# Kernel tuning notes

Measured on AMD Instinct MI355X. Metric: run time of the kernel, lower is better.

The kernel has to match this reference:

```python
import jax, jax.numpy as jnp
import numpy as np

B, T, C, H, E, K = 2, 2048, 1024, 16, 8, 2
HD = C // H  # 64
FF = 4 * C   # 4096


def _ln(x, g, b, eps=1e-5):
    m = x.mean(-1, keepdims=True)
    v = x.var(-1, keepdims=True)
    return (x - m) / jnp.sqrt(v + eps) * g + b


def setup_inputs() -> dict:
    key = jax.random.key(0)
    ks = jax.random.split(key, 12)
    s = 0.02
    return {
        "x": jax.random.normal(ks[0], (B, T, C), jnp.float32),
        "Wq": jax.random.normal(ks[1], (H, C, HD), jnp.float32) * s,
        "Wk": jax.random.normal(ks[2], (H, C, HD), jnp.float32) * s,
        "Wv": jax.random.normal(ks[3], (H, C, HD), jnp.float32) * s,
        "Wo": jax.random.normal(ks[4], (C, C), jnp.float32) * s,
        "bo": jnp.zeros((C,), jnp.float32),
        "ln1_g": jnp.ones((C,), jnp.float32),
        "ln1_b": jnp.zeros((C,), jnp.float32),
        "Wr": jax.random.normal(ks[5], (C, E), jnp.float32) * s,
        "br": jnp.zeros((E,), jnp.float32),
        "Wn": jax.random.normal(ks[6], (C, E), jnp.float32) * s,
        "bn": jnp.zeros((E,), jnp.float32),
        "W1": jax.random.normal(ks[7], (E, C, FF), jnp.float32) * s,
        "b1": jnp.zeros((E, FF), jnp.float32),
        "W2": jax.random.normal(ks[8], (E, FF, C), jnp.float32) * s,
        "b2": jnp.zeros((E, C), jnp.float32),
        "ln2_g": jnp.ones((C,), jnp.float32),
        "ln2_b": jnp.zeros((C,), jnp.float32),
        "noise": jax.random.normal(ks[9], (B, T, E), jnp.float32),
    }


def reference(x, Wq, Wk, Wv, Wo, bo, ln1_g, ln1_b, Wr, br, Wn, bn,
              W1, b1, W2, b2, ln2_g, ln2_b, noise):
    # --- multi-head causal attention (note: scale uses full C, faithful to source) ---
    q = jnp.einsum('btc,hcd->bhtd', x, Wq)
    k = jnp.einsum('btc,hcd->bhtd', x, Wk)
    v = jnp.einsum('btc,hcd->bhtd', x, Wv)
    wei = jnp.einsum('bhtd,bhsd->bhts', q, k) * (C ** -0.5)
    mask = jnp.tril(jnp.ones((T, T), bool))
    wei = jnp.where(mask, wei, -jnp.inf)
    wei = jax.nn.softmax(wei, axis=-1)
    attn = jnp.einsum('bhts,bhsd->bhtd', wei, v)
    attn = attn.transpose(0, 2, 1, 3).reshape(B, T, C)  # concat heads
    attn = attn @ Wo + bo  # proj (dropout = identity in eval)
    x1 = x + _ln(attn, ln1_g, ln1_b)

    # --- noisy top-k router ---
    logits = x1 @ Wr + br                          # [B,T,E]
    noise_logits = x1 @ Wn + bn
    noisy = logits + noise * jax.nn.softplus(noise_logits)
    top_vals, top_idx = jax.lax.top_k(noisy, K)    # [B,T,K]
    # softmax over -inf-filled sparse logits == softmax over the top-k values,
    # scattered back to expert slots; non-selected experts get exactly 0.
    sm = jax.nn.softmax(top_vals, axis=-1)         # [B,T,K]
    gates = jnp.sum(jax.nn.one_hot(top_idx, E, dtype=x.dtype) * sm[..., None], axis=-2)  # [B,T,E]

    # --- experts: dense grouped FFN, combined with (mostly-zero) gates ---
    h = jnp.einsum('btc,ecf->ebtf', x1, W1) + b1[:, None, None, :]
    h = jax.nn.gelu(h, approximate=False)          # torch nn.GELU default = exact erf
    eo = jnp.einsum('ebtf,efc->ebtc', h, W2) + b2[:, None, None, :]
    moe = jnp.einsum('ebtc,bte->btc', eo, gates)

    return x1 + _ln(moe, ln2_g, ln2_b)
```

## Files before the change

### kernel.cpp

```cpp
#include <hip/hip_runtime.h>
#include <math.h>

constexpr int BB = 2, TT = 2048, CC = 1024, HH = 16, HD = 64, EE = 8, FF = 4096;
constexpr int BT = BB * TT;
constexpr int FFC = 2048;

constexpr size_t W = (size_t)BT * CC;
constexpr size_t OFF_Q    = 0;
constexpr size_t OFF_K    = W;
constexpr size_t OFF_V    = 2 * W;
constexpr size_t SM_BASE  = 3 * W;
constexpr size_t SM_GATES = SM_BASE;
constexpr size_t SM_EIDS  = SM_BASE + 8192;
constexpr size_t SM_STOK  = SM_BASE + 16384;
constexpr size_t SM_SGATE = SM_BASE + 24576;
constexpr size_t SM_CNT   = SM_BASE + 32768;
constexpr size_t SM_OFFS  = SM_BASE + 32776;
constexpr size_t SM_CUR   = SM_BASE + 32784;
constexpr size_t SM_ACNT  = SM_BASE + 32792;

typedef short bf16x8 __attribute__((ext_vector_type(8)));
typedef float f32x4  __attribute__((ext_vector_type(4)));

__device__ __forceinline__ float gelu_exact(float v) {
    return 0.5f * v * (1.0f + erff(v * 0.70710678118654752440f));
}

__device__ __forceinline__ short f2bf(float f) {
    unsigned u = __float_as_uint(f);
    unsigned r = 0x7fffu + ((u >> 16) & 1u);
    return (short)((u + r) >> 16);
}

__device__ __forceinline__ bf16x8 pack8(float4 a, float4 b) {
    bf16x8 o;
    o[0] = f2bf(a.x); o[1] = f2bf(a.y); o[2] = f2bf(a.z); o[3] = f2bf(a.w);
    o[4] = f2bf(b.x); o[5] = f2bf(b.y); o[6] = f2bf(b.z); o[7] = f2bf(b.w);
    return o;
}

__device__ __forceinline__ void f4a(float4 v, float* a) {
    a[0] = v.x; a[1] = v.y; a[2] = v.z; a[3] = v.w;
}

__device__ __forceinline__ int SW(int r, int c4) {
    return (((c4 >> 2) ^ ((r >> 2) & 15)) << 2);
}

__device__ __forceinline__ void sgemm128_core(const float* __restrict__ ap,
                                              const float* __restrict__ bp0,
                                              const float* __restrict__ bp1,
                                              long bks, int Kd, float acc[8][8],
                                              float (*As)[128], float (*Bs)[128]) {
    const int t    = threadIdx.x;
    const int kb   = (t & 1) << 3;
    const int mrow = t >> 1;
    const int kq   = t >> 4;
    const int c16  = (t & 15) << 2;
    const int tr4  = (t >> 4) << 2, tc4 = (t & 15) << 2;
    float4 a0 = *(const float4*)(ap + kb);
    float4 a1 = *(const float4*)(ap + kb + 4);
    float4 b0 = *(const float4*)(bp0);
    float4 b1 = *(const float4*)(bp1);
    for (int k0 = 0; k0 < Kd; k0 += 16) {
        __syncthreads();
        As[kb + 0][mrow] = a0.x; As[kb + 1][mrow] = a0.y;
        As[kb + 2][mrow] = a0.z; As[kb + 3][mrow] = a0.w;
        As[kb + 4][mrow] = a1.x; As[kb + 5][mrow] = a1.y;
        As[kb + 6][mrow] = a1.z; As[kb + 7][mrow] = a1.w;
        *(float4*)&Bs[kq][c16]      = b0;
        *(float4*)&Bs[kq][c16 + 64] = b1;
        __syncthreads();
        if (k0 + 16 < Kd) {
            a0 = *(const float4*)(ap + k0 + 16 + kb);
            a1 = *(const float4*)(ap + k0 + 16 + kb + 4);
            b0 = *(const float4*)(bp0 + (size_t)(k0 + 16) * bks);
            b1 = *(const float4*)(bp1 + (size_t)(k0 + 16) * bks);
        }
#pragma unroll
        for (int kk = 0; kk < 16; ++kk) {
            float av[8], bv[8];
            f4a(*(const float4*)&As[kk][tr4],      av);
            f4a(*(const float4*)&As[kk][tr4 + 64], av + 4);
            f4a(*(const float4*)&Bs[kk][tc4],      bv);
            f4a(*(const float4*)&Bs[kk][tc4 + 64], bv + 4);
#pragma unroll
            for (int i = 0; i < 8; ++i)
#pragma unroll
                for (int j = 0; j < 8; ++j)
                    acc[i][j] = fmaf(av[i], bv[j], acc[i][j]);
        }
    }
}

__global__ __launch_bounds__(256) void qkv_kernel(const float* __restrict__ x,
                                                  const float* __restrict__ Wq,
                                                  const float* __restrict__ Wk,
                                                  const float* __restrict__ Wv,
                                                  float* __restrict__ q,
                                                  float* __restrict__ k,
                                                  float* __restrict__ v) {
    __shared__ float As[16][128], Bs[16][128];
    const int mt = blockIdx.x, nt = blockIdx.y, wz = blockIdx.z;
    const float* Wm = (wz == 0) ? Wq : ((wz == 1) ? Wk : Wv);
    float* out = (wz == 0) ? q : ((wz == 1) ? k : v);
    const int t = threadIdx.x;
    const int kq = t >> 4, c16 = (t & 15) << 2;
    const float* ap  = x + (size_t)(mt * 128 + (t >> 1)) * CC;
    const float* bp0 = Wm + ((size_t)(2 * nt)     * CC + kq) * HD + c16;
    const float* bp1 = Wm + ((size_t)(2 * nt + 1) * CC + kq) * HD + c16;
    float acc[8][8] = {};
    sgemm128_core(ap, bp0, bp1, HD, CC, acc, As, Bs);
    const int tr4 = (t >> 4) << 2, tc4 = (t & 15) << 2;
#pragma unroll
    for (int i = 0; i < 8; ++i) {
        const int row = mt * 128 + (i >> 2) * 64 + tr4 + (i & 3);
        float4 o0, o1;
        o0.x = acc[i][0]; o0.y = acc[i][1]; o0.z = acc[i][2]; o0.w = acc[i][3];
        o1.x = acc[i][4]; o1.y = acc[i][5]; o1.z = acc[i][6]; o1.w = acc[i][7];
        *(float4*)&out[(size_t)row * CC + nt * 128 + tc4]      = o0;
        *(float4*)&out[(size_t)row * CC + nt * 128 + 64 + tc4] = o1;
    }
}

__global__ __launch_bounds__(256) void gemm_bias_kernel(const float* __restrict__ A,
                                                        const float* __restrict__ Bm,
                                                        const float* __restrict__ bias,
                                                        float* __restrict__ out,
                                                        int N, int Kd) {
    __shared__ float As[16][128], Bs[16][128];
    const int mt = blockIdx.x, nt = blockIdx.y;
    const int t = threadIdx.x;
    const int kq = t >> 4, c16 = (t & 15) << 2;
    const float* ap  = A + (size_t)(mt * 128 + (t >> 1)) * Kd;
    const float* bp0 = Bm + (size_t)kq * N + nt * 128 + c16;
    const float* bp1 = bp0 + 64;
    float acc[8][8] = {};
    sgemm128_core(ap, bp0, bp1, N, Kd, acc, As, Bs);
    const int tr4 = (t >> 4) << 2, tc4 = (t & 15) << 2;
    const float4 ba = *(const float4*)&bias[nt * 128 + tc4];
    const float4 bb = *(const float4*)&bias[nt * 128 + 64 + tc4];
#pragma unroll
    for (int i = 0; i < 8; ++i) {
        const int row = mt * 128 + (i >> 2) * 64 + tr4 + (i & 3);
        float4 o0, o1;
        o0.x = acc[i][0] + ba.x; o0.y = acc[i][1] + ba.y;
        o0.z = acc[i][2] + ba.z; o0.w = acc[i][3] + ba.w;
        o1.x = acc[i][4] + bb.x; o1.y = acc[i][5] + bb.y;
        o1.z = acc[i][6] + bb.z; o1.w = acc[i][7] + bb.w;
        *(float4*)&out[(size_t)row * N + nt * 128 + tc4]      = o0;
        *(float4*)&out[(size_t)row * N + nt * 128 + 64 + tc4] = o1;
    }
}

constexpr int ATTN_JOBS = (TT / 64) * HH * BB;
__global__ __launch_bounds__(256) void attn_kernel(float* __restrict__ q,
                                                   const float* __restrict__ kbuf,
                                                   const float* __restrict__ vbuf,
                                                   int* __restrict__ jctr) {
    __shared__ float Qs[64][64];
    __shared__ float Ks[64][64];
    __shared__ float Vs[64][64];
    __shared__ int jid_s;
    float (*Ps)[64] = Ks;
    const int t = threadIdx.x;
    const int tc4 = (t & 15) << 2, tr4 = (t >> 4) << 2;
    for (;;) {
        __syncthreads();
        if (t == 0) jid_s = atomicAdd(jctr, 1);
        __syncthreads();
        const int jid = jid_s;
        if (jid >= ATTN_JOBS) break;
        const int qt    = (TT / 64 - 1) - (jid >> 5);
        const int plane = jid & 31;
        const int h = plane & 15, b = plane >> 4;
        const size_t base = ((size_t)b * TT) * CC + h * HD;
#pragma unroll
        for (int it = 0; it < 4; ++it) {
            int fi = t + it * 256;
            int r = fi >> 4, c4 = (fi & 15) << 2;
            *(float4*)&Qs[r][SW(r, c4)] =
                *(const float4*)&q[base + (size_t)(qt * 64 + r) * CC + c4];
        }
        float4 kr[4], vr[4];
#pragma unroll
        for (int it = 0; it < 4; ++it) {
            int fi = t + it * 256;
            int s = fi >> 4, c4 = (fi & 15) << 2;
            kr[it] = *(const float4*)&kbuf[base + (size_t)s * CC + c4];
            vr[it] = *(const float4*)&vbuf[base + (size_t)s * CC + c4];
        }
        float o[4][4] = {};
        float m_r[4], l_r[4];
#pragma unroll
        for (int i = 0; i < 4; ++i) { m_r[i] = -INFINITY; l_r[i] = 0.0f; }

        for (int kt = 0; kt <= qt; ++kt) {
            __syncthreads();
#pragma unroll
            for (int it = 0; it < 4; ++it) {
                int fi = t + it * 256;
                int s = fi >> 4, c4 = (fi & 15) << 2;
                *(float4*)&Ks[s][SW(s, c4)] = kr[it];
                *(float4*)&Vs[s][SW(s, c4)] = vr[it];
            }
            __syncthreads();
            if (kt < qt) {
#pragma unroll
                for (int it = 0; it < 4; ++it) {
                    int fi = t + it * 256;
                    int s = fi >> 4, c4 = (fi & 15) << 2;
                    kr[it] = *(const float4*)&kbuf[base + (size_t)((kt + 1) * 64 + s) * CC + c4];
                    vr[it] = *(const float4*)&vbuf[base + (size_t)((kt + 1) * 64 + s) * CC + c4];
                }
            }
            float s4[4][4] = {};
            for (int d4 = 0; d4 < 64; d4 += 4) {
                float qa[4][4], ka[4][4];
#pragma unroll
                for (int i = 0; i < 4; ++i)
                    f4a(*(const float4*)&Qs[tr4 + i][SW(tr4 + i, d4)], qa[i]);
#pragma unroll
                for (int j = 0; j < 4; ++j)
                    f4a(*(const float4*)&Ks[tc4 + j][SW(tc4 + j, d4)], ka[j]);
#pragma unroll
                for (int i = 0; i < 4; ++i)
#pragma unroll
                    for (int j = 0; j < 4; ++j) {
                        float a = s4[i][j];
                        a = fmaf(qa[i][0], ka[j][0], a);
                        a = fmaf(qa[i][1], ka[j][1], a);
                        a = fmaf(qa[i][2], ka[j][2], a);
                        a = fmaf(qa[i][3], ka[j][3], a);
                        s4[i][j] = a;
                    }
            }
            const float scale = 0.03125f;
#pragma unroll
            for (int i = 0; i < 4; ++i)
#pragma unroll
                for (int j = 0; j < 4; ++j) {
                    float sv = s4[i][j] * scale;
                    if (kt == qt && (tc4 + j) > (tr4 + i)) sv = -INFINITY;
                    s4[i][j] = sv;
                }
            float p4[4][4];
#pragma unroll
            for (int i = 0; i < 4; ++i) {
                float mt_i = fmaxf(fmaxf(s4[i][0], s4[i][1]), fmaxf(s4[i][2], s4[i][3]));
#pragma unroll
                for (int msk = 1; msk <= 8; msk <<= 1) mt_i = fmaxf(mt_i, __shfl_xor(mt_i, msk, 64));
                float m_new = fmaxf(m_r[i], mt_i);
                float alpha = expf(m_r[i] - m_new);
                float ls = 0.0f;
#pragma unroll
                for (int j = 0; j < 4; ++j) {
                    float p = expf(s4[i][j] - m_new);
                    p4[i][j] = p;
                    ls += p;
                }
#pragma unroll
                for (int msk = 1; msk <= 8; msk <<= 1) ls += __shfl_xor(ls, msk, 64);
                l_r[i] = l_r[i] * alpha + ls;
                m_r[i] = m_new;
#pragma unroll
                for (int j = 0; j < 4; ++j) o[i][j] *= alpha;
            }
            __syncthreads();
#pragma unroll
            for (int i = 0; i < 4; ++i) {
                float4 pv;
                pv.x = p4[i][0]; pv.y = p4[i][1]; pv.z = p4[i][2]; pv.w = p4[i][3];
                *(float4*)&Ps[tr4 + i][SW(tr4 + i, tc4)] = pv;
            }
            __syncthreads();
            for (int s0 = 0; s0 < 64; s0 += 4) {
                float pa[4][4], va[4][4];
#pragma unroll
                for (int i = 0; i < 4; ++i)
                    f4a(*(const float4*)&Ps[tr4 + i][SW(tr4 + i, s0)], pa[i]);
#pragma unroll
                for (int qq = 0; qq < 4; ++qq)
                    f4a(*(const float4*)&Vs[s0 + qq][SW(s0 + qq, tc4)], va[qq]);
#pragma unroll
                for (int i = 0; i < 4; ++i)
#pragma unroll
                    for (int j = 0; j < 4; ++j) {
                        float a = o[i][j];
                        a = fmaf(pa[i][0], va[0][j], a);
                        a = fmaf(pa[i][1], va[1][j], a);
                        a = fmaf(pa[i][2], va[2][j], a);
                        a = fmaf(pa[i][3], va[3][j], a);
                        o[i][j] = a;
                    }
            }
        }
#pragma unroll
        for (int i = 0; i < 4; ++i) {
            const float inv = 1.0f / l_r[i];
            float4 o4;
            o4.x = o[i][0] * inv; o4.y = o[i][1] * inv; o4.z = o[i][2] * inv; o4.w = o[i][3] * inv;
            *(float4*)&q[base + (size_t)(qt * 64 + tr4 + i) * CC + tc4] = o4;
        }
    }
}

__device__ __forceinline__ void compute_step(short (*As)[40], short (*Bs)[40],
                                             f32x4 acc[4][4], int wm, int wn,
                                             int l15, int q8) {
    bf16x8 a[4], b[4];
#pragma unroll
    for (int i = 0; i < 4; ++i) a[i] = *(bf16x8*)&As[wm + i * 16 + l15][q8];
#pragma unroll
    for (int j = 0; j < 4; ++j) b[j] = *(bf16x8*)&Bs[wn + j * 16 + l15][q8];
#pragma unroll
    for (int i = 0; i < 4; ++i)
#pragma unroll
        for (int j = 0; j < 4; ++j)
            acc[i][j] = __builtin_amdgcn_mfma_f32_16x16x32_bf16(a[i], b[j], acc[i][j], 0, 0, 0);
}

#define MM_PROLOG                                                    \
    const int t = threadIdx.x, lane = t & 63, wid = t >> 6;          \
    const int wm = (wid >> 1) * 64, wn = (wid & 1) * 64;             \
    const int l15 = lane & 15, q8 = (lane >> 4) * 8;                 \
    const int arow = t >> 1, akh = (t & 1) * 16;                     \
    const int bn = t & 127, bkh = (t >> 7) * 16;

__global__ __launch_bounds__(256) void mm_ffn1(const float* __restrict__ x1,
                                               const float* __restrict__ W1,
                                               const float* __restrict__ b1,
                                               const int* __restrict__ stok,
                                               const int* __restrict__ offs,
                                               const int* __restrict__ cnt,
                                               short* __restrict__ hbuf, int fbase) {
    __shared__ short As[128][40], Bs[128][40];
    const int e = blockIdx.z, mt = blockIdx.x, nt = blockIdx.y;
    const int ne = cnt[e];
    if (mt * 128 >= ne) return;
    MM_PROLOG
    const int off_e = offs[e];
    int rl = mt * 128 + arow;
    if (rl >= ne) rl = ne - 1;
    const int token = stok[off_e + rl];
    const float* ap = x1 + (size_t)token * CC;
    const float* bp = W1 + (size_t)e * CC * FF + fbase + nt * 128 + bn;
    f32x4 acc[4][4] = {};
    float4 apf[4];
    float bpf[16];
#pragma unroll
    for (int qd = 0; qd < 4; ++qd) apf[qd] = *(const float4*)(ap + akh + 4 * qd);
#pragma unroll
    for (int kk = 0; kk < 16; ++kk) bpf[kk] = bp[(size_t)(bkh + kk) * FF];
    for (int k0 = 0; k0 < CC; k0 += 32) {
        __syncthreads();
        *(bf16x8*)&As[arow][akh]     = pack8(apf[0], apf[1]);
        *(bf16x8*)&As[arow][akh + 8] = pack8(apf[2], apf[3]);
        {
            bf16x8 o0, o1;
#pragma unroll
            for (int kk = 0; kk < 8; ++kk) { o0[kk] = f2bf(bpf[kk]); o1[kk] = f2bf(bpf[kk + 8]); }
            *(bf16x8*)&Bs[bn][bkh]     = o0;
            *(bf16x8*)&Bs[bn][bkh + 8] = o1;
        }
        __syncthreads();
        if (k0 + 32 < CC) {
#pragma unroll
            for (int qd = 0; qd < 4; ++qd)
                apf[qd] = *(const float4*)(ap + k0 + 32 + akh + 4 * qd);
#pragma unroll
            for (int kk = 0; kk < 16; ++kk)
                bpf[kk] = bp[(size_t)(k0 + 32 + bkh + kk) * FF];
        }
        compute_step(As, Bs, acc, wm, wn, l15, q8);
    }
    float bj[4];
#pragma unroll
    for (int j = 0; j < 4; ++j)
        bj[j] = b1[(size_t)e * FF + fbase + nt * 128 + wn + j * 16 + l15];
    const int colb = nt * 128 + wn;
#pragma unroll
    for (int i = 0; i < 4; ++i) {
#pragma unroll
        for (int r = 0; r < 4; ++r) {
            const int row = mt * 128 + wm + i * 16 + (lane >> 4) * 4 + r;
            if (row < ne) {
                short* orow = hbuf + (size_t)(off_e + row) * FFC + colb;
#pragma unroll
                for (int j = 0; j < 4; ++j)
                    orow[j * 16 + l15] = f2bf(gelu_exact(acc[i][j][r] + bj[j]));
            }
        }
    }
}

__global__ __launch_bounds__(256) void mm_ffn2(const short* __restrict__ hbuf,
                                               const float* __restrict__ W2,
                                               const float* __restrict__ b2,
                                               const int* __restrict__ stok,
                                               const float* __restrict__ sgate,
                                               const int* __restrict__ offs,
                                               const int* __restrict__ cnt,
                                               float* __restrict__ moe,
                                               int fbase, int first) {
    __shared__ short As[128][40], Bs[128][40];
    const int e = blockIdx.z, mt = blockIdx.x, nt = blockIdx.y;
    const int ne = cnt[e];
    if (mt * 128 >= ne) return;
    MM_PROLOG
    const int off_e = offs[e];
    int rl = mt * 128 + arow;
    if (rl >= ne) rl = ne - 1;
    const short* ap = hbuf + (size_t)(off_e + rl) * FFC;
    const float* bp = W2 + (size_t)e * FF * CC + (size_t)fbase * CC + nt * 128 + bn;
    f32x4 acc[4][4] = {};
    bf16x8 a0pf = *(const bf16x8*)(ap + akh);
    bf16x8 a1pf = *(const bf16x8*)(ap + akh + 8);
    float bpf[16];
#pragma unroll
    for (int kk = 0; kk < 16; ++kk) bpf[kk] = bp[(size_t)(bkh + kk) * CC];
    for (int k0 = 0; k0 < FFC; k0 += 32) {
        __syncthreads();
        *(bf16x8*)&As[arow][akh]     = a0pf;
        *(bf16x8*)&As[arow][akh + 8] = a1pf;
        {
            bf16x8 o0, o1;
#pragma unroll
            for (int kk = 0; kk < 8; ++kk) { o0[kk] = f2bf(bpf[kk]); o1[kk] = f2bf(bpf[kk + 8]); }
            *(bf16x8*)&Bs[bn][bkh]     = o0;
            *(bf16x8*)&Bs[bn][bkh + 8] = o1;
        }
        __syncthreads();
        if (k0 + 32 < FFC) {
            a0pf = *(const bf16x8*)(ap + k0 + 32 + akh);
            a1pf = *(const bf16x8*)(ap + k0 + 32 + akh + 8);
#pragma unroll
            for (int kk = 0; kk < 16; ++kk)
                bpf[kk] = bp[(size_t)(k0 + 32 + bkh + kk) * CC];
        }
        compute_step(As, Bs, acc, wm, wn, l15, q8);
    }
    float bj[4];
    int colj[4];
#pragma unroll
    for (int j = 0; j < 4; ++j) {
        colj[j] = nt * 128 + wn + j * 16 + l15;
        bj[j] = first ? b2[(size_t)e * CC + colj[j]] : 0.0f;
    }
#pragma unroll
    for (int i = 0; i < 4; ++i) {
#pragma unroll
        for (int r = 0; r < 4; ++r) {
            const int row = mt * 128 + wm + i * 16 + (lane >> 4) * 4 + r;
            if (row < ne) {
                const int slot = off_e + row;
                const int token = stok[slot];
                const float g = sgate[slot];
                float* dst = moe + (size_t)token * CC;
#pragma unroll
                for (int j = 0; j < 4; ++j)
                    atomicAdd(dst + colj[j], g * (acc[i][j][r] + bj[j]));
            }
        }
    }
}

__device__ __forceinline__ float block_sum(float v, float* red) {
#pragma unroll
    for (int m = 32; m >= 1; m >>= 1) v += __shfl_xor(v, m, 64);
    const int w = threadIdx.x >> 6;
    __syncthreads();
    if ((threadIdx.x & 63) == 0) red[w] = v;
    __syncthreads();
    return red[0] + red[1] + red[2] + red[3];
}

__global__ __launch_bounds__(256) void ln_res_kernel(const float* __restrict__ src,
                                                     const float* __restrict__ res,
                                                     const float* __restrict__ gam,
                                                     const float* __restrict__ bet,
                                                     float* __restrict__ out) {
    __shared__ float red[4];
    const int row = blockIdx.x, t = threadIdx.x;
    const float4 sv = *(const float4*)&src[(size_t)row * CC + t * 4];
    const float total = block_sum(sv.x + sv.y + sv.z + sv.w, red);
    const float mean = total * (1.0f / CC);
    const float d0 = sv.x - mean, d1 = sv.y - mean, d2 = sv.z - mean, d3 = sv.w - mean;
    const float var = block_sum(d0 * d0 + d1 * d1 + d2 * d2 + d3 * d3, red) * (1.0f / CC);
    const float rstd = rsqrtf(var + 1e-5f);
    const float4 rv = *(const float4*)&res[(size_t)row * CC + t * 4];
    const float4 g4 = *(const float4*)&gam[t * 4];
    const float4 b4 = *(const float4*)&bet[t * 4];
    float4 o4;
    o4.x = rv.x + d0 * rstd * g4.x + b4.x;
    o4.y = rv.y + d1 * rstd * g4.y + b4.y;
    o4.z = rv.z + d2 * rstd * g4.z + b4.z;
    o4.w = rv.w + d3 * rstd * g4.w + b4.w;
    *(float4*)&out[(size_t)row * CC + t * 4] = o4;
}

__global__ __launch_bounds__(256) void router_kernel(const float* __restrict__ x1,
                                                     const float* __restrict__ Wr,
                                                     const float* __restrict__ br,
                                                     const float* __restrict__ Wn,
                                                     const float* __restrict__ bn,
                                                     const float* __restrict__ noise,
                                                     float* __restrict__ gates,
                                                     int* __restrict__ eids,
                                                     int* __restrict__ counts) {
    __shared__ float xs[CC];
    __shared__ float part[256];
    __shared__ float dots[16];
    const int tk = blockIdx.x, t = threadIdx.x;
    *(float4*)&xs[t * 4] = *(const float4*)&x1[(size_t)tk * CC + t * 4];
    __syncthreads();
    const int o = t & 15, cs = t >> 4;
    float acc = 0.0f;
    if (o < 8) {
        for (int c = cs; c < CC; c += 16) acc += xs[c] * Wr[c * EE + o];
    } else {
        const int e = o - 8;
        for (int c = cs; c < CC; c += 16) acc += xs[c] * Wn[c * EE + e];
    }
    part[t] = acc;
    __syncthreads();
    if (t < 16) {
        float s = 0.0f;
        for (int i = 0; i < 16; ++i) s += part[t + 16 * i];
        dots[t] = s;
    }
    __syncthreads();
    if (t == 0) {
        float noisy[EE];
        for (int e = 0; e < EE; ++e) {
            const float lg = dots[e] + br[e];
            const float nl = dots[8 + e] + bn[e];
            const float sp = fmaxf(nl, 0.0f) + log1pf(expf(-fabsf(nl)));
            noisy[e] = lg + noise[(size_t)tk * EE + e] * sp;
        }
        int e1 = 0; float v1 = noisy[0];
        for (int e = 1; e < EE; ++e) if (noisy[e] > v1) { v1 = noisy[e]; e1 = e; }
        int e2 = -1; float v2 = -INFINITY;
        for (int e = 0; e < EE; ++e) if (e != e1 && noisy[e] > v2) { v2 = noisy[e]; e2 = e; }
        const float ex = expf(v2 - v1);
        const float inv = 1.0f / (1.0f + ex);
        gates[2 * tk] = inv; gates[2 * tk + 1] = ex * inv;
        eids[2 * tk] = e1; eids[2 * tk + 1] = e2;
        atomicAdd(&counts[e1], 1);
        atomicAdd(&counts[e2], 1);
    }
}

__global__ void zero_counts_kernel(int* __restrict__ cnt, int* __restrict__ acnt) {
    if (threadIdx.x < EE) cnt[threadIdx.x] = 0;
    if (threadIdx.x == EE) *acnt = 0;
}

__global__ void offsets_kernel(const int* __restrict__ cnt, int* __restrict__ offs,
                               int* __restrict__ cur) {
    const int t = threadIdx.x;
    if (t == 0) {
        int a = 0;
        for (int e = 0; e < EE; ++e) { offs[e] = a; a += cnt[e]; }
    }
    if (t < EE) cur[t] = 0;
}

__global__ __launch_bounds__(256) void scatter_kernel(const int* __restrict__ eids,
                                                      const float* __restrict__ gates,
                                                      int* __restrict__ cur,
                                                      const int* __restrict__ offs,
                                                      int* __restrict__ slot_token,
                                                      float* __restrict__ slot_gate) {
    const int tk = blockIdx.x * 256 + threadIdx.x;
    if (tk >= BT) return;
#pragma unroll
    for (int ki = 0; ki < 2; ++ki) {
        const int e = eids[2 * tk + ki];
        const int idx = atomicAdd(&cur[e], 1);
        const int slot = offs[e] + idx;
        slot_token[slot] = tk;
        slot_gate[slot] = gates[2 * tk + ki];
    }
}

__global__ __launch_bounds__(256) void zero_kernel(float* __restrict__ p, int n4) {
    const int i = blockIdx.x * 256 + threadIdx.x;
    if (i < n4) ((float4*)p)[i] = make_float4(0.f, 0.f, 0.f, 0.f);
}

extern "C" void kernel_launch(void* const* d_in, const int* in_sizes, int n_in,
                              void* d_out, int out_size, void* d_ws, size_t ws_size,
                              hipStream_t stream) {
    (void)in_sizes; (void)n_in; (void)out_size; (void)ws_size;
    const float* x    = (const float*)d_in[0];
    const float* Wq   = (const float*)d_in[1];
    const float* Wk   = (const float*)d_in[2];
    const float* Wv   = (const float*)d_in[3];
    const float* Wo   = (const float*)d_in[4];
    const float* bo   = (const float*)d_in[5];
    const float* ln1g = (const float*)d_in[6];
    const float* ln1b = (const float*)d_in[7];
    const float* Wr   = (const float*)d_in[8];
    const float* br   = (const float*)d_in[9];
    const float* Wn   = (const float*)d_in[10];
    const float* bn   = (const float*)d_in[11];
    const float* W1   = (const float*)d_in[12];
    const float* b1   = (const float*)d_in[13];
    const float* W2   = (const float*)d_in[14];
    const float* b2   = (const float*)d_in[15];
    const float* ln2g = (const float*)d_in[16];
    const float* ln2b = (const float*)d_in[17];
    const float* noise= (const float*)d_in[18];
    float* out = (float*)d_out;
    float* ws  = (float*)d_ws;
    int*   iws = (int*)d_ws;

    float* qb    = ws + OFF_Q;
    float* kb    = ws + OFF_K;
    float* vb    = ws + OFF_V;
    float* proj  = ws + OFF_V;
    float* x1    = out;
    short* hbuf  = (short*)(ws + OFF_Q);
    float* moe   = ws + OFF_V;
    float* gates = ws + SM_GATES;
    float* sgate = ws + SM_SGATE;
    int* eids  = iws + SM_EIDS;
    int* stok  = iws + SM_STOK;
    int* cnt   = iws + SM_CNT;
    int* offs  = iws + SM_OFFS;
    int* cur   = iws + SM_CUR;
    int* acnt  = iws + SM_ACNT;

    zero_counts_kernel<<<1, 64, 0, stream>>>(cnt, acnt);
    qkv_kernel<<<dim3(BT / 128, CC / 128, 3), 256, 0, stream>>>(x, Wq, Wk, Wv, qb, kb, vb);
    attn_kernel<<<dim3(768), 256, 0, stream>>>(qb, kb, vb, acnt);
    gemm_bias_kernel<<<dim3(BT / 128, CC / 128), 256, 0, stream>>>(qb, Wo, bo, proj, CC, CC);
    ln_res_kernel<<<BT, 256, 0, stream>>>(proj, x, ln1g, ln1b, x1);
    router_kernel<<<BT, 256, 0, stream>>>(x1, Wr, br, Wn, bn, noise, gates, eids, cnt);
    offsets_kernel<<<1, 64, 0, stream>>>(cnt, offs, cur);
    scatter_kernel<<<BT / 256, 256, 0, stream>>>(eids, gates, cur, offs, stok, sgate);
    zero_kernel<<<(BT * CC / 4 + 255) / 256, 256, 0, stream>>>(moe, BT * CC / 4);
    for (int ccnk = 0; ccnk < FF / FFC; ++ccnk) {
        mm_ffn1<<<dim3(2 * BT / 128, FFC / 128, EE), 256, 0, stream>>>(
            x1, W1, b1, stok, offs, cnt, hbuf, ccnk * FFC);
        mm_ffn2<<<dim3(2 * BT / 128, CC / 128, EE), 256, 0, stream>>>(
            hbuf, W2, b2, stok, sgate, offs, cnt, moe, ccnk * FFC, ccnk == 0 ? 1 : 0);
    }
    ln_res_kernel<<<BT, 256, 0, stream>>>(moe, x1, ln2g, ln2b, out);
}
```

Measured before the change: 2.499 ms.

## Replace atomic scatter-add with per-slot expert output and fused gated combine+LN

The second FFN GEMM now writes its output per routed slot into a dense buffer (store on the first chunk, read-modify-write on later chunks) instead of atomically adding gated results into per-token rows. A new combine kernel gathers each token's two slot rows, applies the gates, and fuses LayerNorm plus residual, so the zero-fill kernel goes away. The scatter kernel records each token's slot indices in place of its expert ids. The FF chunk size is halved to 1024, which doubles the number of GEMM launches and the read-modify-write passes over the expert-output buffer.

```diff
diff --git a/kernel.cpp b/kernel.cpp
--- a/kernel.cpp
+++ b/kernel.cpp
@@ -3,7 +3,7 @@
 
 constexpr int BB = 2, TT = 2048, CC = 1024, HH = 16, HD = 64, EE = 8, FF = 4096;
 constexpr int BT = BB * TT;
-constexpr int FFC = 2048;
+constexpr int FFC = 1024;
 
 constexpr size_t W = (size_t)BT * CC;
 constexpr size_t OFF_Q    = 0;
@@ -397,11 +397,9 @@
 __global__ __launch_bounds__(256) void mm_ffn2(const short* __restrict__ hbuf,
                                                const float* __restrict__ W2,
                                                const float* __restrict__ b2,
-                                               const int* __restrict__ stok,
-                                               const float* __restrict__ sgate,
                                                const int* __restrict__ offs,
                                                const int* __restrict__ cnt,
-                                               float* __restrict__ moe,
+                                               float* __restrict__ eo,
                                                int fbase, int first) {
     __shared__ short As[128][40], Bs[128][40];
     const int e = blockIdx.z, mt = blockIdx.x, nt = blockIdx.y;
@@ -453,13 +451,16 @@
         for (int r = 0; r < 4; ++r) {
             const int row = mt * 128 + wm + i * 16 + (lane >> 4) * 4 + r;
             if (row < ne) {
-                const int slot = off_e + row;
-                const int token = stok[slot];
-                const float g = sgate[slot];
-                float* dst = moe + (size_t)token * CC;
-#pragma unroll
-                for (int j = 0; j < 4; ++j)
-                    atomicAdd(dst + colj[j], g * (acc[i][j][r] + bj[j]));
+                float* dst = eo + (size_t)(off_e + row) * CC;
+                if (first) {
+#pragma unroll
+                    for (int j = 0; j < 4; ++j)
+                        dst[colj[j]] = acc[i][j][r] + bj[j];
+                } else {
+#pragma unroll
+                    for (int j = 0; j < 4; ++j)
+                        dst[colj[j]] += acc[i][j][r];
+                }
             }
         }
     }
@@ -499,6 +500,40 @@
     *(float4*)&out[(size_t)row * CC + t * 4] = o4;
 }
 
+__global__ __launch_bounds__(256) void combine_ln_kernel(const float* __restrict__ eo,
+                                                         const int* __restrict__ tslot,
+                                                         const float* __restrict__ gates,
+                                                         const float* __restrict__ res,
+                                                         const float* __restrict__ gam,
+                                                         const float* __restrict__ bet,
+                                                         float* __restrict__ out) {
+    __shared__ float red[4];
+    const int tk = blockIdx.x, t = threadIdx.x;
+    const int s0 = tslot[2 * tk], s1 = tslot[2 * tk + 1];
+    const float g0 = gates[2 * tk], g1 = gates[2 * tk + 1];
+    const float4 a = *(const float4*)&eo[(size_t)s0 * CC + t * 4];
+    const float4 b = *(const float4*)&eo[(size_t)s1 * CC + t * 4];
+    float4 sv;
+    sv.x = g0 * a.x + g1 * b.x;
+    sv.y = g0 * a.y + g1 * b.y;
+    sv.z = g0 * a.z + g1 * b.z;
+    sv.w = g0 * a.w + g1 * b.w;
+    const float total = block_sum(sv.x + sv.y + sv.z + sv.w, red);
+    const float mean = total * (1.0f / CC);
+    const float d0 = sv.x - mean, d1 = sv.y - mean, d2 = sv.z - mean, d3 = sv.w - mean;
+    const float var = block_sum(d0 * d0 + d1 * d1 + d2 * d2 + d3 * d3, red) * (1.0f / CC);
+    const float rstd = rsqrtf(var + 1e-5f);
+    const float4 rv = *(const float4*)&res[(size_t)tk * CC + t * 4];
+    const float4 g4 = *(const float4*)&gam[t * 4];
+    const float4 b4 = *(const float4*)&bet[t * 4];
+    float4 o4;
+    o4.x = rv.x + d0 * rstd * g4.x + b4.x;
+    o4.y = rv.y + d1 * rstd * g4.y + b4.y;
+    o4.z = rv.z + d2 * rstd * g4.z + b4.z;
+    o4.w = rv.w + d3 * rstd * g4.w + b4.w;
+    *(float4*)&out[(size_t)tk * CC + t * 4] = o4;
+}
+
 __global__ __launch_bounds__(256) void router_kernel(const float* __restrict__ x1,
                                                      const float* __restrict__ Wr,
                                                      const float* __restrict__ br,
@@ -566,7 +601,7 @@
     if (t < EE) cur[t] = 0;
 }
 
-__global__ __launch_bounds__(256) void scatter_kernel(const int* __restrict__ eids,
+__global__ __launch_bounds__(256) void scatter_kernel(int* __restrict__ eids_tslot,
                                                       const float* __restrict__ gates,
                                                       int* __restrict__ cur,
                                                       const int* __restrict__ offs,
@@ -576,17 +611,13 @@
     if (tk >= BT) return;
 #pragma unroll
     for (int ki = 0; ki < 2; ++ki) {
-        const int e = eids[2 * tk + ki];
+        const int e = eids_tslot[2 * tk + ki];
         const int idx = atomicAdd(&cur[e], 1);
         const int slot = offs[e] + idx;
         slot_token[slot] = tk;
         slot_gate[slot] = gates[2 * tk + ki];
-    }
-}
-
-__global__ __launch_bounds__(256) void zero_kernel(float* __restrict__ p, int n4) {
-    const int i = blockIdx.x * 256 + threadIdx.x;
-    if (i < n4) ((float4*)p)[i] = make_float4(0.f, 0.f, 0.f, 0.f);
+        eids_tslot[2 * tk + ki] = slot;
+    }
 }
 
 extern "C" void kernel_launch(void* const* d_in, const int* in_sizes, int n_in,
@@ -622,7 +653,7 @@
     float* proj  = ws + OFF_V;
     float* x1    = out;
     short* hbuf  = (short*)(ws + OFF_Q);
-    float* moe   = ws + OFF_V;
+    float* eo    = ws + OFF_K;
     float* gates = ws + SM_GATES;
     float* sgate = ws + SM_SGATE;
     int* eids  = iws + SM_EIDS;
@@ -640,12 +671,11 @@
     router_kernel<<<BT, 256, 0, stream>>>(x1, Wr, br, Wn, bn, noise, gates, eids, cnt);
     offsets_kernel<<<1, 64, 0, stream>>>(cnt, offs, cur);
     scatter_kernel<<<BT / 256, 256, 0, stream>>>(eids, gates, cur, offs, stok, sgate);
-    zero_kernel<<<(BT * CC / 4 + 255) / 256, 256, 0, stream>>>(moe, BT * CC / 4);
     for (int ccnk = 0; ccnk < FF / FFC; ++ccnk) {
         mm_ffn1<<<dim3(2 * BT / 128, FFC / 128, EE), 256, 0, stream>>>(
             x1, W1, b1, stok, offs, cnt, hbuf, ccnk * FFC);
         mm_ffn2<<<dim3(2 * BT / 128, CC / 128, EE), 256, 0, stream>>>(
-            hbuf, W2, b2, stok, sgate, offs, cnt, moe, ccnk * FFC, ccnk == 0 ? 1 : 0);
-    }
-    ln_res_kernel<<<BT, 256, 0, stream>>>(moe, x1, ln2g, ln2b, out);
-}
+            hbuf, W2, b2, offs, cnt, eo, ccnk * FFC, ccnk == 0 ? 1 : 0);
+    }
+    combine_ln_kernel<<<BT, 256, 0, stream>>>(eo, eids, gates, x1, ln2g, ln2b, out);
+}
```

After: 2.583 ms. 3.4% more time.
